# Performance work log

Measured on AMD Instinct MI355X. Metric: run time of the kernel, lower is better.

The kernel has to match this reference:

```python
import jax, jax.numpy as jnp
import numpy as np
from jax import lax

# QuantumDMRGLayer (isolated_labelnode=True) as a pure MPS chain contraction.
# Per sample: contract each site's (2,m[,m]) tensor with the 2-dim input vector
# over the physical leg, then multiply the resulting bond matrices along the
# chain, inserting the (m,m,nblabels) output tensor after site pos_label.

B, L, M, NBL = 2048, 196, 16, 10  # batch, dimvec, bond_len, nblabels


def setup_inputs() -> dict:
    key = jax.random.key(0)
    k_in, k_mid, k_l, k_r, k_out = jax.random.split(key, 5)
    # std chosen for numerical stability of a 196-long matrix product:
    # each site matrix is x0*A[0]+x1*A[1] with x~N(0,1), so effective per-site
    # gain ~ std*sqrt(2*m); std = 1/sqrt(2*m) keeps the product O(1).
    std = 1.0 / np.sqrt(2.0 * M)
    inputs = jax.random.normal(k_in, (B, L, 2), dtype=jnp.float32)
    eye2m = jnp.eye(M, dtype=jnp.float32)[:2, :]  # eye(max(2,m))[0:2,:] -> (2, m)
    A_left = eye2m + 1e-3 * jax.random.normal(k_l, (2, M), dtype=jnp.float32)
    A_right = eye2m + 1e-3 * jax.random.normal(k_r, (2, M), dtype=jnp.float32)
    A_mid = std * jax.random.normal(k_mid, (L - 2, 2, M, M), dtype=jnp.float32)
    T_out = (1.0 / np.sqrt(M)) * jax.random.normal(k_out, (M, M, NBL), dtype=jnp.float32)
    return {
        "inputs": inputs,
        "A_left": A_left,
        "A_mid": A_mid,
        "A_right": A_right,
        "T_out": T_out,
        "pos_label": 98,
    }


def reference(inputs, A_left, A_mid, A_right, T_out, pos_label):
    # Contract physical legs: interior site i (1..L-2) -> batched (m,m) matrix.
    mats = jnp.einsum("bsd,sdij->sbij", inputs[:, 1:-1, :], A_mid)  # (L-2, B, m, m)
    v_left = jnp.einsum("bd,dm->bm", inputs[:, 0, :], A_left)       # (B, m)
    v_right = jnp.einsum("bd,dm->bm", inputs[:, -1, :], A_right)    # (B, m)

    def step_l(v, Mx):  # v @ M, batched
        return jnp.einsum("bm,bmn->bn", v, Mx), None

    def step_r(v, Mx):  # M @ v, batched (sweep from the right end inward)
        return jnp.einsum("bmn,bn->bm", Mx, v), None

    # sites 1..pos_label feed the left bond of the output node,
    # sites pos_label+1..L-2 feed the right bond.
    left, _ = lax.scan(step_l, v_left, mats[:pos_label])
    right, _ = lax.scan(step_r, v_right, mats[pos_label:], reverse=True)
    return jnp.einsum("bm,mnl,bn->bl", left, T_out, right)  # (B, nblabels)
```

## Files before the change

### kernel.cpp

```cpp
#include <hip/hip_runtime.h>


typedef __attribute__((ext_vector_type(8))) short short8;
typedef __attribute__((ext_vector_type(16))) float floatx16;

#define GSITE_DW 512
#define GDIR_DW (100 * GSITE_DW)

__device__ __forceinline__ unsigned bf16_rne(unsigned u) {
    return (u + 0x7FFFu + ((u >> 16) & 1u)) >> 16;
}

__global__ __launch_bounds__(256)
void prep_kernel(const float* __restrict__ AM, unsigned* __restrict__ WS)
{
    int t = blockIdx.x * 256 + threadIdx.x;
    const int w    = t & 3;  t >>= 2;
    const int lane = t & 63; t >>= 6;
    const int p    = t % 100;
    const int dir  = t / 100;
    const int kb = (lane >> 5) << 3;
    const int r  = lane & 31;
    const int rr = (r & 0x13) | ((r & 4) << 1) | ((r & 8) >> 1);
    const int d = rr >> 4, nn = rr & 15;
    const int lim = dir ? 96 : 98;
    const int a = dir ? (193 - p) : p;
    const int k0 = kb + 2 * w;
    float g0 = 0.f, g1 = 0.f;
    if (p < lim) {
        const float* Ab = AM + a * 512 + d * 256;
        if (dir == 0) { g0 = Ab[k0 * 16 + nn]; g1 = Ab[(k0 + 1) * 16 + nn]; }
        else          { g0 = Ab[nn * 16 + k0]; g1 = Ab[nn * 16 + k0 + 1]; }
    }
    const unsigned u0 = __float_as_uint(g0), u1 = __float_as_uint(g1);
    const unsigned h0 = bf16_rne(u0), h1 = bf16_rne(u1);
    const float l0f = g0 - __uint_as_float(h0 << 16);
    const float l1f = g1 - __uint_as_float(h1 << 16);
    const unsigned lo0 = bf16_rne(__float_as_uint(l0f));
    const unsigned lo1 = bf16_rne(__float_as_uint(l1f));
    unsigned* gp = WS + (dir * 100 + p) * GSITE_DW;
    gp[lane * 4 + w]       = (h1 << 16) | h0;
    gp[256 + lane * 4 + w] = (lo1 << 16) | lo0;
}

__global__ __launch_bounds__(512, 4)
void fused_kernel(const float* __restrict__ X,
                  const float* __restrict__ AL,
                  const float* __restrict__ AR,
                  const float* __restrict__ T,
                  const unsigned* __restrict__ WS,
                  float* __restrict__ OUT)
{
    __shared__ float sT[2560];
    __shared__ float sS[8][4][16][17];
    __shared__ float sv[4][2][16];

    const int tid  = threadIdx.x;
    const int lane = tid & 63;
    const int wv   = tid >> 6;
    for (int k = tid; k < 640; k += 512)
        ((float4*)sT)[k] = ((const float4*)T)[k];

    const int dir = wv >> 2;
    const int si  = wv & 3;
    int p0, p1;
    if (dir == 0) { p0 = (si < 2) ? 25 * si : 50 + 24 * (si - 2);
                    p1 = p0 + ((si < 2) ? 25 : 24); }
    else          { p0 = 24 * si; p1 = p0 + 24; }

    const int sel = (lane >> 4) & 1;
    const int m   = lane & 15;
    const int kb  = (lane >> 5) << 3;
    const int sb  = blockIdx.x * 4;
    const float* Xs0 = X + (sb + sel) * 392;
    const float* Xs1 = X + (sb + 2 + sel) * 392;
    const unsigned* Gb = WS + dir * GDIR_DW + lane * 4;

    float w0[8], w1[8];
    int4 vh0, vl0, vh1, vl1;
#pragma unroll
    for (int j = 0; j < 8; ++j) w0[j] = (kb + j == m) ? 1.0f : 0.0f;
#pragma unroll
    for (int q = 0; q < 4; ++q) {
        const unsigned h0 = __float_as_uint(w0[2 * q]) & 0xFFFF0000u;
        const unsigned h1 = __float_as_uint(w0[2 * q + 1]) & 0xFFFF0000u;
        ((unsigned*)&vh0)[q] = h1 | (h0 >> 16);
        ((unsigned*)&vl0)[q] = 0;
        w1[2 * q] = w0[2 * q]; w1[2 * q + 1] = w0[2 * q + 1];
    }
    vh1 = vh0; vl1 = vl0;

    auto comb = [&](const floatx16& D, const float2 xs,
                    float* wq, int4& vh, int4& vl) {
#pragma unroll
        for (int q = 0; q < 4; ++q) {
            const float a0 = fmaf(xs.x, D[2 * q],     xs.y * D[2 * q + 8]);
            const float a1 = fmaf(xs.x, D[2 * q + 1], xs.y * D[2 * q + 9]);
            wq[2 * q] = a0; wq[2 * q + 1] = a1;
            const unsigned u0 = __float_as_uint(a0);
            const unsigned u1 = __float_as_uint(a1);
            const float l0 = a0 - __uint_as_float(u0 & 0xFFFF0000u);
            const float l1 = a1 - __uint_as_float(u1 & 0xFFFF0000u);
            ((unsigned*)&vh)[q] = __builtin_amdgcn_perm(u1, u0, 0x07060302u);
            ((unsigned*)&vl)[q] = __builtin_amdgcn_perm(
                __float_as_uint(l1), __float_as_uint(l0), 0x07060302u);
        }
    };

    int4 GH[2], GL[2];
    float2 xr0[2], xr1[2];
#pragma unroll
    for (int i = 0; i < 2; ++i) {
        const int p = p0 + i;
        GH[i] = *(const int4*)(Gb + p * GSITE_DW);
        GL[i] = *(const int4*)(Gb + p * GSITE_DW + 256);
        const int xo = dir ? (388 - 2 * p) : (2 + 2 * p);
        xr0[i] = *(const float2*)(Xs0 + xo);
        xr1[i] = *(const float2*)(Xs1 + xo);
    }

    for (int c = 0; c < 14; ++c) {
#pragma unroll
        for (int j2 = 0; j2 < 2; ++j2) {
            const int p = p0 + 2 * c + j2;
            if (p < p1) {
                const short8 ah  = *(const short8*)&GH[j2];
                const short8 al  = *(const short8*)&GL[j2];
                const short8 bh0 = *(const short8*)&vh0;
                const short8 bl0 = *(const short8*)&vl0;
                floatx16 D0 = {};
                D0 = __builtin_amdgcn_mfma_f32_32x32x16_bf16(ah, bh0, D0, 0, 0, 0);
                D0 = __builtin_amdgcn_mfma_f32_32x32x16_bf16(ah, bl0, D0, 0, 0, 0);
                D0 = __builtin_amdgcn_mfma_f32_32x32x16_bf16(al, bh0, D0, 0, 0, 0);
                comb(D0, xr0[j2], w0, vh0, vl0);
                const short8 bh1 = *(const short8*)&vh1;
                const short8 bl1 = *(const short8*)&vl1;
                floatx16 D1 = {};
                D1 = __builtin_amdgcn_mfma_f32_32x32x16_bf16(ah, bh1, D1, 0, 0, 0);
                D1 = __builtin_amdgcn_mfma_f32_32x32x16_bf16(ah, bl1, D1, 0, 0, 0);
                D1 = __builtin_amdgcn_mfma_f32_32x32x16_bf16(al, bh1, D1, 0, 0, 0);
                comb(D1, xr1[j2], w1, vh1, vl1);
            }
            int pn = p + 2;
            if (pn >= p1) pn = 99;
            GH[j2] = *(const int4*)(Gb + pn * GSITE_DW);
            GL[j2] = *(const int4*)(Gb + pn * GSITE_DW + 256);
            const int xo = dir ? (388 - 2 * pn) : (2 + 2 * pn);
            xr0[j2] = *(const float2*)(Xs0 + xo);
            xr1[j2] = *(const float2*)(Xs1 + xo);
        }
    }

#pragma unroll
    for (int j = 0; j < 8; ++j) {
        sS[wv][sel][kb + j][m]     = w0[j];
        sS[wv][2 + sel][kb + j][m] = w1[j];
    }
    __syncthreads();

    if (wv < 2) {
        const int smp   = wv * 2 + (lane >> 5);
        const int chain = (lane >> 4) & 1;
        const int n     = lane & 15;
        const float2 x  = *(const float2*)(X + (sb + smp) * 392 +
                                           (chain ? 390 : 0));
        const float* Ab = chain ? AR : AL;
        float v = x.x * Ab[n] + x.y * Ab[16 + n];
#pragma unroll
        for (int q = 0; q < 4; ++q) {
            const float* Srow = &sS[chain * 4 + q][smp][n][0];
            float acc = 0.f;
#pragma unroll
            for (int mm = 0; mm < 16; ++mm)
                acc = fmaf(Srow[mm], __shfl(v, mm, 16), acc);
            v = acc;
        }
        sv[smp][chain][n] = v;

        if (lane < 20) {
            const int s2 = lane / 10, l = lane - s2 * 10;
            const int sm = wv * 2 + s2;
            const float* Lp = sv[sm][0];
            const float* Rp = sv[sm][1];
            float acc = 0.f;
#pragma unroll
            for (int mm = 0; mm < 16; ++mm) {
                const float lm = Lp[mm];
                const float* Tp = sT + mm * 160 + l;
#pragma unroll
                for (int nn = 0; nn < 16; ++nn)
                    acc = fmaf(lm * Rp[nn], Tp[nn * 10], acc);
            }
            OUT[(sb + sm) * 10 + l] = acc;
        }
    }
}

extern "C" void kernel_launch(void* const* d_in, const int* in_sizes, int n_in,
                              void* d_out, int out_size, void* d_ws, size_t ws_size,
                              hipStream_t stream)
{
    const float* X  = (const float*)d_in[0];
    const float* AL = (const float*)d_in[1];
    const float* AM = (const float*)d_in[2];
    const float* AR = (const float*)d_in[3];
    const float* T  = (const float*)d_in[4];
    (void)in_sizes; (void)n_in; (void)out_size; (void)ws_size;
    unsigned* WS = (unsigned*)d_ws;
    float* OUT   = (float*)d_out;

    hipLaunchKernelGGL(prep_kernel,  dim3(200), dim3(256), 0, stream, AM, WS);
    hipLaunchKernelGGL(fused_kernel, dim3(512), dim3(512), 0, stream,
                       X, AL, AR, T, WS, OUT);
}
```

Measured before the change: 94.40 us.

## Split chain into segment kernel with LDS-staged site tensors and separate combine kernel

Replaces the fused kernel with two kernels. The segment kernel stages one segment's bf16 hi/lo site tensors and the matching inputs into shared memory, then each wave runs that segment's chain product for two samples across 32 samples per block. The per-segment matrices go through global workspace to a combine kernel, which applies the boundary vectors and the output tensor. This trades the old per-wave global loads of site tensors for LDS reuse across many samples. It adds one kernel launch and a global round-trip for the segment matrices, and processes only one sample pair per wave per step, where the old code interleaved two.

Result: slower. 99.69 us (+5.6%).

```diff
diff --git a/kernel.cpp b/kernel.cpp
--- a/kernel.cpp
+++ b/kernel.cpp
@@ -6,6 +6,7 @@
 
 #define GSITE_DW 512
 #define GDIR_DW (100 * GSITE_DW)
+#define S_OFF_DW (2 * GDIR_DW)
 
 __device__ __forceinline__ unsigned bf16_rne(unsigned u) {
     return (u + 0x7FFFu + ((u >> 16) & 1u)) >> 16;
@@ -43,156 +44,155 @@
     gp[256 + lane * 4 + w] = (lo1 << 16) | lo0;
 }
 
-__global__ __launch_bounds__(512, 4)
-void fused_kernel(const float* __restrict__ X,
-                  const float* __restrict__ AL,
-                  const float* __restrict__ AR,
-                  const float* __restrict__ T,
-                  const unsigned* __restrict__ WS,
-                  float* __restrict__ OUT)
-{
-    __shared__ float sT[2560];
-    __shared__ float sS[8][4][16][17];
-    __shared__ float sv[4][2][16];
+__global__ __launch_bounds__(1024, 4)
+void seg_kernel(const float* __restrict__ X,
+                const unsigned* __restrict__ WS,
+                float* __restrict__ S)
+{
+    __shared__ unsigned sG[25 * GSITE_DW];
+    __shared__ float2 sxv[32][25];
 
     const int tid  = threadIdx.x;
     const int lane = tid & 63;
     const int wv   = tid >> 6;
-    for (int k = tid; k < 640; k += 512)
-        ((float4*)sT)[k] = ((const float4*)T)[k];
-
-    const int dir = wv >> 2;
-    const int si  = wv & 3;
+    const int seg  = blockIdx.x & 7;
+    const int sb   = (blockIdx.x >> 3) * 32;
+    const int dir  = seg >> 2;
+    const int si   = seg & 3;
     int p0, p1;
     if (dir == 0) { p0 = (si < 2) ? 25 * si : 50 + 24 * (si - 2);
                     p1 = p0 + ((si < 2) ? 25 : 24); }
     else          { p0 = 24 * si; p1 = p0 + 24; }
+    const int len = p1 - p0;
+
+    const int4* gsrc = (const int4*)(WS + (dir * 100 + p0) * GSITE_DW);
+    const int n4 = len * 128;
+    for (int i = tid; i < n4; i += 1024)
+        ((int4*)sG)[i] = gsrc[i];
+    for (int i = tid; i < 32 * 25; i += 1024) {
+        const int smp = i / 25, li = i - smp * 25;
+        if (li < len) {
+            const int p = p0 + li;
+            const int xo = dir ? (388 - 2 * p) : (2 + 2 * p);
+            sxv[smp][li] = *(const float2*)(X + (sb + smp) * 392 + xo);
+        }
+    }
+    __syncthreads();
 
     const int sel = (lane >> 4) & 1;
     const int m   = lane & 15;
     const int kb  = (lane >> 5) << 3;
-    const int sb  = blockIdx.x * 4;
-    const float* Xs0 = X + (sb + sel) * 392;
-    const float* Xs1 = X + (sb + 2 + sel) * 392;
-    const unsigned* Gb = WS + dir * GDIR_DW + lane * 4;
-
-    float w0[8], w1[8];
-    int4 vh0, vl0, vh1, vl1;
-#pragma unroll
-    for (int j = 0; j < 8; ++j) w0[j] = (kb + j == m) ? 1.0f : 0.0f;
+    const int s   = sb + 2 * wv + sel;
+
+    int4 vh, vl;
 #pragma unroll
     for (int q = 0; q < 4; ++q) {
-        const unsigned h0 = __float_as_uint(w0[2 * q]) & 0xFFFF0000u;
-        const unsigned h1 = __float_as_uint(w0[2 * q + 1]) & 0xFFFF0000u;
-        ((unsigned*)&vh0)[q] = h1 | (h0 >> 16);
-        ((unsigned*)&vl0)[q] = 0;
-        w1[2 * q] = w0[2 * q]; w1[2 * q + 1] = w0[2 * q + 1];
-    }
-    vh1 = vh0; vl1 = vl0;
-
-    auto comb = [&](const floatx16& D, const float2 xs,
-                    float* wq, int4& vh, int4& vl) {
-#pragma unroll
-        for (int q = 0; q < 4; ++q) {
-            const float a0 = fmaf(xs.x, D[2 * q],     xs.y * D[2 * q + 8]);
-            const float a1 = fmaf(xs.x, D[2 * q + 1], xs.y * D[2 * q + 9]);
-            wq[2 * q] = a0; wq[2 * q + 1] = a1;
-            const unsigned u0 = __float_as_uint(a0);
-            const unsigned u1 = __float_as_uint(a1);
-            const float l0 = a0 - __uint_as_float(u0 & 0xFFFF0000u);
-            const float l1 = a1 - __uint_as_float(u1 & 0xFFFF0000u);
-            ((unsigned*)&vh)[q] = __builtin_amdgcn_perm(u1, u0, 0x07060302u);
-            ((unsigned*)&vl)[q] = __builtin_amdgcn_perm(
-                __float_as_uint(l1), __float_as_uint(l0), 0x07060302u);
+        unsigned hw = 0;
+        if (kb + 2 * q == m)     hw |= 0x3F80u;
+        if (kb + 2 * q + 1 == m) hw |= 0x3F800000u;
+        ((unsigned*)&vh)[q] = hw;
+        ((unsigned*)&vl)[q] = 0;
+    }
+
+    const unsigned* Gl = sG + lane * 4;
+    int4 GHc = *(const int4*)(Gl);
+    int4 GLc = *(const int4*)(Gl + 256);
+    float2 xc = sxv[2 * wv + sel][0];
+    float w[8];
+    for (int q = 0; q < len; ++q) {
+        const int qn = (q + 1 < len) ? q + 1 : q;
+        const int4 GHn = *(const int4*)(Gl + qn * GSITE_DW);
+        const int4 GLn = *(const int4*)(Gl + qn * GSITE_DW + 256);
+        const float2 xn = sxv[2 * wv + sel][qn];
+
+        const short8 ah = *(const short8*)&GHc;
+        const short8 al = *(const short8*)&GLc;
+        const short8 bh = *(const short8*)&vh;
+        const short8 bl = *(const short8*)&vl;
+        floatx16 D = {};
+        D = __builtin_amdgcn_mfma_f32_32x32x16_bf16(ah, bh, D, 0, 0, 0);
+        D = __builtin_amdgcn_mfma_f32_32x32x16_bf16(ah, bl, D, 0, 0, 0);
+        D = __builtin_amdgcn_mfma_f32_32x32x16_bf16(al, bh, D, 0, 0, 0);
+#pragma unroll
+        for (int j = 0; j < 8; ++j)
+            w[j] = fmaf(xc.x, D[j], xc.y * D[j + 8]);
+        if (q + 1 < len) {
+#pragma unroll
+            for (int qq = 0; qq < 4; ++qq) {
+                const unsigned u0 = __float_as_uint(w[2 * qq]);
+                const unsigned u1 = __float_as_uint(w[2 * qq + 1]);
+                const float l0 = w[2 * qq]     - __uint_as_float(u0 & 0xFFFF0000u);
+                const float l1 = w[2 * qq + 1] - __uint_as_float(u1 & 0xFFFF0000u);
+                ((unsigned*)&vh)[qq] = __builtin_amdgcn_perm(u1, u0, 0x07060302u);
+                ((unsigned*)&vl)[qq] = __builtin_amdgcn_perm(
+                    __float_as_uint(l1), __float_as_uint(l0), 0x07060302u);
+            }
         }
-    };
-
-    int4 GH[2], GL[2];
-    float2 xr0[2], xr1[2];
-#pragma unroll
-    for (int i = 0; i < 2; ++i) {
-        const int p = p0 + i;
-        GH[i] = *(const int4*)(Gb + p * GSITE_DW);
-        GL[i] = *(const int4*)(Gb + p * GSITE_DW + 256);
-        const int xo = dir ? (388 - 2 * p) : (2 + 2 * p);
-        xr0[i] = *(const float2*)(Xs0 + xo);
-        xr1[i] = *(const float2*)(Xs1 + xo);
-    }
-
-    for (int c = 0; c < 14; ++c) {
-#pragma unroll
-        for (int j2 = 0; j2 < 2; ++j2) {
-            const int p = p0 + 2 * c + j2;
-            if (p < p1) {
-                const short8 ah  = *(const short8*)&GH[j2];
-                const short8 al  = *(const short8*)&GL[j2];
-                const short8 bh0 = *(const short8*)&vh0;
-                const short8 bl0 = *(const short8*)&vl0;
-                floatx16 D0 = {};
-                D0 = __builtin_amdgcn_mfma_f32_32x32x16_bf16(ah, bh0, D0, 0, 0, 0);
-                D0 = __builtin_amdgcn_mfma_f32_32x32x16_bf16(ah, bl0, D0, 0, 0, 0);
-                D0 = __builtin_amdgcn_mfma_f32_32x32x16_bf16(al, bh0, D0, 0, 0, 0);
-                comb(D0, xr0[j2], w0, vh0, vl0);
-                const short8 bh1 = *(const short8*)&vh1;
-                const short8 bl1 = *(const short8*)&vl1;
-                floatx16 D1 = {};
-                D1 = __builtin_amdgcn_mfma_f32_32x32x16_bf16(ah, bh1, D1, 0, 0, 0);
-                D1 = __builtin_amdgcn_mfma_f32_32x32x16_bf16(ah, bl1, D1, 0, 0, 0);
-                D1 = __builtin_amdgcn_mfma_f32_32x32x16_bf16(al, bh1, D1, 0, 0, 0);
-                comb(D1, xr1[j2], w1, vh1, vl1);
-            }
-            int pn = p + 2;
-            if (pn >= p1) pn = 99;
-            GH[j2] = *(const int4*)(Gb + pn * GSITE_DW);
-            GL[j2] = *(const int4*)(Gb + pn * GSITE_DW + 256);
-            const int xo = dir ? (388 - 2 * pn) : (2 + 2 * pn);
-            xr0[j2] = *(const float2*)(Xs0 + xo);
-            xr1[j2] = *(const float2*)(Xs1 + xo);
+        GHc = GHn; GLc = GLn; xc = xn;
+    }
+
+    float* Sp = S + ((seg * 2048 + s) << 8) + m;
+#pragma unroll
+    for (int j = 0; j < 8; ++j)
+        Sp[(kb + j) << 4] = w[j];
+}
+
+__global__ __launch_bounds__(256)
+void comb_kernel(const float* __restrict__ X,
+                 const float* __restrict__ AL,
+                 const float* __restrict__ AR,
+                 const float* __restrict__ T,
+                 const float* __restrict__ S,
+                 float* __restrict__ OUT)
+{
+    __shared__ float sT[2560];
+    __shared__ float sv[8][2][16];
+    const int tid = threadIdx.x;
+    for (int k = tid; k < 640; k += 256)
+        ((float4*)sT)[k] = ((const float4*)T)[k];
+
+    const int g     = tid >> 4;
+    const int n     = tid & 15;
+    const int smp   = g >> 1;
+    const int chain = g & 1;
+    const int s     = blockIdx.x * 8 + smp;
+
+    float4 r[4][4];
+#pragma unroll
+    for (int q = 0; q < 4; ++q) {
+        const float4* Ps =
+            (const float4*)(S + (((chain * 4 + q) * 2048 + s) << 8) + (n << 4));
+        r[q][0] = Ps[0]; r[q][1] = Ps[1]; r[q][2] = Ps[2]; r[q][3] = Ps[3];
+    }
+    const float2 x = *(const float2*)(X + s * 392 + (chain ? 390 : 0));
+    const float* Ab = chain ? AR : AL;
+    float v = x.x * Ab[n] + x.y * Ab[16 + n];
+#pragma unroll
+    for (int q = 0; q < 4; ++q) {
+        float acc = 0.f;
+#pragma unroll
+        for (int mm = 0; mm < 16; ++mm)
+            acc = fmaf(((const float*)&r[q][mm >> 2])[mm & 3],
+                       __shfl(v, mm, 16), acc);
+        v = acc;
+    }
+    sv[smp][chain][n] = v;
+    __syncthreads();
+
+    if (tid < 80) {
+        const int s2 = tid / 10, l = tid - s2 * 10;
+        const float* Lp = sv[s2][0];
+        const float* Rp = sv[s2][1];
+        float acc = 0.f;
+#pragma unroll
+        for (int mm = 0; mm < 16; ++mm) {
+            const float lm = Lp[mm];
+            const float* Tp = sT + mm * 160 + l;
+#pragma unroll
+            for (int nn = 0; nn < 16; ++nn)
+                acc = fmaf(lm * Rp[nn], Tp[nn * 10], acc);
         }
-    }
-
-#pragma unroll
-    for (int j = 0; j < 8; ++j) {
-        sS[wv][sel][kb + j][m]     = w0[j];
-        sS[wv][2 + sel][kb + j][m] = w1[j];
-    }
-    __syncthreads();
-
-    if (wv < 2) {
-        const int smp   = wv * 2 + (lane >> 5);
-        const int chain = (lane >> 4) & 1;
-        const int n     = lane & 15;
-        const float2 x  = *(const float2*)(X + (sb + smp) * 392 +
-                                           (chain ? 390 : 0));
-        const float* Ab = chain ? AR : AL;
-        float v = x.x * Ab[n] + x.y * Ab[16 + n];
-#pragma unroll
-        for (int q = 0; q < 4; ++q) {
-            const float* Srow = &sS[chain * 4 + q][smp][n][0];
-            float acc = 0.f;
-#pragma unroll
-            for (int mm = 0; mm < 16; ++mm)
-                acc = fmaf(Srow[mm], __shfl(v, mm, 16), acc);
-            v = acc;
-        }
-        sv[smp][chain][n] = v;
-
-        if (lane < 20) {
-            const int s2 = lane / 10, l = lane - s2 * 10;
-            const int sm = wv * 2 + s2;
-            const float* Lp = sv[sm][0];
-            const float* Rp = sv[sm][1];
-            float acc = 0.f;
-#pragma unroll
-            for (int mm = 0; mm < 16; ++mm) {
-                const float lm = Lp[mm];
-                const float* Tp = sT + mm * 160 + l;
-#pragma unroll
-                for (int nn = 0; nn < 16; ++nn)
-                    acc = fmaf(lm * Rp[nn], Tp[nn * 10], acc);
-            }
-            OUT[(sb + sm) * 10 + l] = acc;
-        }
+        OUT[(blockIdx.x * 8 + s2) * 10 + l] = acc;
     }
 }
 
@@ -207,9 +207,11 @@
     const float* T  = (const float*)d_in[4];
     (void)in_sizes; (void)n_in; (void)out_size; (void)ws_size;
     unsigned* WS = (unsigned*)d_ws;
+    float* S     = (float*)d_ws + S_OFF_DW;
     float* OUT   = (float*)d_out;
 
-    hipLaunchKernelGGL(prep_kernel,  dim3(200), dim3(256), 0, stream, AM, WS);
-    hipLaunchKernelGGL(fused_kernel, dim3(512), dim3(512), 0, stream,
-                       X, AL, AR, T, WS, OUT);
-}
+    hipLaunchKernelGGL(prep_kernel, dim3(200), dim3(256),  0, stream, AM, WS);
+    hipLaunchKernelGGL(seg_kernel,  dim3(512), dim3(1024), 0, stream, X, WS, S);
+    hipLaunchKernelGGL(comb_kernel, dim3(256), dim3(256),  0, stream,
+                       X, AL, AR, T, S, OUT);
+}
```
